# Kernel tuning notes

Measured on AMD Instinct MI355X. Metric: run time of the kernel, lower is better.

Reference implementation:

```python
import jax, jax.numpy as jnp
import numpy as np

PI = float(np.pi)
BN_EPS = 1e-3
LN_EPS = 1e-5


def ssslu(x, shape, bias):
    # x * (sin(softsign(x) * shape*pi/2) + (bias + 1))
    s = x / (1.0 + jnp.abs(x))
    return x * (jnp.sin(s * (shape * PI / 2.0)) + (bias + 1.0))


def bn(x, g, b, m, v):
    inv = (g / jnp.sqrt(v + BN_EPS))[None, :, None, None]
    return (x - m[None, :, None, None]) * inv + b[None, :, None, None]


def conv2d(x, w, bias=None, pad=0):
    y = jax.lax.conv_general_dilated(x, w, (1, 1), [(pad, pad), (pad, pad)],
                                     dimension_numbers=('NCHW', 'OIHW', 'NCHW'))
    if bias is not None:
        y = y + bias[None, :, None, None]
    return y


def ln_silu(v):
    # LayerNorm (unit weight, zero bias) over last axis, then SiLU
    mu = jnp.mean(v, axis=-1, keepdims=True)
    var = jnp.mean(jnp.square(v - mu), axis=-1, keepdims=True)
    h = (v - mu) / jnp.sqrt(var + LN_EPS)
    return h * jax.nn.sigmoid(h)


def _forward(x, w_qkv, g_qkv, b_qkv, m_qkv, v_qkv,
             w_co, g_co, b_co, m_co, v_co,
             w_b1, bias_b1, g_b1, b_b1, m_b1, v_b1,
             w_b2, bias_b2, g_b2, b_b2, m_b2, v_b2):
    B, C, H, W = x.shape
    Q = (w_qkv.shape[0] - C) // 2
    # qkv Conv block: conv1x1 -> SSSLU(-3, 0.3) -> BN
    t = bn(ssslu(conv2d(x, w_qkv, pad=0), -3.0, 0.3), g_qkv, b_qkv, m_qkv, v_qkv)
    xq, xk, xv = jnp.split(t, [Q, 2 * Q], axis=1)
    # max-pooled Q/K rows and columns -> [B*Q, W] / [B*Q, H]
    qw = jnp.max(xq, axis=2).reshape(B * Q, W)
    kw = jnp.max(xk, axis=2).reshape(B * Q, W)
    qh = jnp.max(xq, axis=3).reshape(B * Q, H)
    kh = jnp.max(xk, axis=3).reshape(B * Q, H)
    # xaw[i,b] = max_a qw[i,a]*kw[i,b]; xah[i,a] = max_b qh[i,a]*kh[i,b]
    xaw = jnp.max(qw[:, :, None] * kw[:, None, :], axis=1)  # [BQ, W]
    xah = jnp.max(qh[:, :, None] * kh[:, None, :], axis=2)  # [BQ, H]
    xaw = ln_silu(xaw)
    xah = ln_silu(xah)
    xa = (xah[:, :, None] * xaw[:, None, :]).reshape(B, Q, H, W)
    # co: SSSLUConv(Q+C -> Q): conv3x3 -> BN -> SSSLU(1.0, 0)
    xa = jnp.concatenate([xa, xv], axis=1)
    xa = ssslu(bn(conv2d(xa, w_co, pad=1), g_co, b_co, m_co, v_co), 1.0, 0.0)
    # back[0]: Conv(Q -> C, k3, bias): conv -> SSSLU(-3, 0.3) -> BN
    xa = bn(ssslu(conv2d(xa, w_b1, bias_b1, pad=1), -3.0, 0.3), g_b1, b_b1, m_b1, v_b1)
    # back[1]: SSSLUConv(C -> C, k1, bias): conv -> BN -> SSSLU(0.8, 0)
    xa = ssslu(bn(conv2d(xa, w_b2, bias_b2, pad=0), g_b2, b_b2, m_b2, v_b2), 0.8, 0.0)
    # back[2]: Sigmoid; source returns the gate itself
    return jax.nn.sigmoid(xa)


def setup_inputs() -> dict:
    B, C, Q, H, W = 16, 256, 256, 64, 64
    key = jax.random.key(0)
    ks = jax.random.split(key, 32)

    def w_init(k, o, i, kh, kw):
        return jax.random.normal(k, (o, i, kh, kw), jnp.float32) * (1.0 / np.sqrt(i * kh * kw))

    def bn_params(k, c):
        k1, k2, k3, k4 = jax.random.split(k, 4)
        g = jax.random.uniform(k1, (c,), jnp.float32, 0.5, 1.5)
        b = jax.random.normal(k2, (c,), jnp.float32) * 0.1
        m = jax.random.normal(k3, (c,), jnp.float32) * 0.1
        v = jax.random.uniform(k4, (c,), jnp.float32, 0.5, 1.5)
        return g, b, m, v

    x = jax.random.normal(ks[0], (B, C, H, W), jnp.float32)
    w_qkv = w_init(ks[1], 2 * Q + C, C, 1, 1)
    g_qkv, b_qkv, m_qkv, v_qkv = bn_params(ks[2], 2 * Q + C)
    w_co = w_init(ks[3], Q, Q + C, 3, 3)
    g_co, b_co, m_co, v_co = bn_params(ks[4], Q)
    w_b1 = w_init(ks[5], C, Q, 3, 3)
    bias_b1 = jax.random.normal(ks[6], (C,), jnp.float32) * 0.05
    g_b1, b_b1, m_b1, v_b1 = bn_params(ks[7], C)
    w_b2 = w_init(ks[8], C, C, 1, 1)
    bias_b2 = jax.random.normal(ks[9], (C,), jnp.float32) * 0.05
    g_b2, b_b2, m_b2, v_b2 = bn_params(ks[10], C)
    return dict(x=x, w_qkv=w_qkv, g_qkv=g_qkv, b_qkv=b_qkv, m_qkv=m_qkv, v_qkv=v_qkv,
                w_co=w_co, g_co=g_co, b_co=b_co, m_co=m_co, v_co=v_co,
                w_b1=w_b1, bias_b1=bias_b1, g_b1=g_b1, b_b1=b_b1, m_b1=m_b1, v_b1=v_b1,
                w_b2=w_b2, bias_b2=bias_b2, g_b2=g_b2, b_b2=b_b2, m_b2=m_b2, v_b2=v_b2)


def reference(x, w_qkv, g_qkv, b_qkv, m_qkv, v_qkv,
              w_co, g_co, b_co, m_co, v_co,
              w_b1, bias_b1, g_b1, b_b1, m_b1, v_b1,
              w_b2, bias_b2, g_b2, b_b2, m_b2, v_b2):
    return _forward(x, w_qkv, g_qkv, b_qkv, m_qkv, v_qkv,
                    w_co, g_co, b_co, m_co, v_co,
                    w_b1, bias_b1, g_b1, b_b1, m_b1, v_b1,
                    w_b2, bias_b2, g_b2, b_b2, m_b2, v_b2)
```

## Files before the change

kernel.cpp:

```cpp
#include <hip/hip_runtime.h>
#include <hip/hip_bf16.h>
#include <math.h>

#define PI_F 3.14159265358979323846f

typedef unsigned short u16;
typedef unsigned int   u32;
typedef float    f32x4 __attribute__((ext_vector_type(4)));
typedef _Float16 f16x8 __attribute__((ext_vector_type(8)));
typedef u16      u16x8 __attribute__((ext_vector_type(8)));
typedef u16      u16x4 __attribute__((ext_vector_type(4)));

__device__ __forceinline__ u16 f2h(float f){ union{ _Float16 h; u16 u; } c; c.h = (_Float16)f; return c.u; }
__device__ __forceinline__ float h2f(u16 u){ union{ u16 u; _Float16 h; } c; c.u = u; return (float)c.h; }

__device__ __forceinline__ void gl16(const void* g, void* l){
  __builtin_amdgcn_global_load_lds((const __attribute__((address_space(1))) u32*)g,
                                   (__attribute__((address_space(3))) u32*)l, 16, 0, 0);
}

__device__ __forceinline__ int SWZ(int r){ return (r>>1)&3; }

__device__ __forceinline__ float wred_max(float v){
#pragma unroll
  for (int m = 32; m; m >>= 1) v = fmaxf(v, __shfl_xor(v, m));
  return v;
}
__device__ __forceinline__ float wred_min(float v){
#pragma unroll
  for (int m = 32; m; m >>= 1) v = fminf(v, __shfl_xor(v, m));
  return v;
}
__device__ __forceinline__ float wred_sum(float v){
#pragma unroll
  for (int m = 32; m; m >>= 1) v += __shfl_xor(v, m);
  return v;
}

__device__ __forceinline__ float ssslu_f(float x, float shp, float bp1){
  float s = x / (1.0f + fabsf(x));
  return x * (__sinf(s * shp) + bp1);
}

__device__ __forceinline__ float epi_val(float v, float4 p, float shp, float bp1, int ORDER, bool SIG){
  v += p.w;
  if (ORDER == 0){ v = ssslu_f(v, shp, bp1); v = (v - p.z) * p.x + p.y; }
  else           { v = (v - p.z) * p.x + p.y; v = ssslu_f(v, shp, bp1); }
  if (SIG) v = 1.f / (1.f + __expf(-v));
  return v;
}

__device__ __forceinline__ f16x8 mul8h(u16x8 a, u16x8 b){
  union{ u16x8 u; f16x8 h; } A, B; A.u = a; B.u = b;
  return A.h * B.h;
}

__global__ __launch_bounds__(256)
void xpose_k(const float* __restrict__ X, u16* __restrict__ XH)
{
  __shared__ u16 L[16384];
  const int tid = threadIdx.x;
  const int b = blockIdx.x >> 6, h = blockIdx.x & 63;
  const float* xp = X + (size_t)b * 256 * 4096 + h * 64;
#pragma unroll
  for (int i = 0; i < 16; ++i){
    int ci = i * 16 + (tid >> 4);
    int w4 = (tid & 15) * 4;
    float4 v = *(const float4*)(xp + (size_t)ci * 4096 + w4);
    int sw = 4 * ((ci >> 3) & 15);
    u16x4 d;
    d[0] = f2h(v.x); d[1] = f2h(v.y); d[2] = f2h(v.z); d[3] = f2h(v.w);
    *(u16x4*)&L[ci * 64 + (w4 ^ sw)] = d;
  }
  __syncthreads();
  u16* out = XH + (((size_t)b * 4096 + (size_t)h * 64) << 8);
#pragma unroll
  for (int it = 0; it < 8; ++it){
    int w   = it * 8 + (tid >> 5);
    int m   = tid & 31;
    int ci0 = m * 8;
    int base = (w & ~3) ^ (4 * (m & 15));
    int wl   = w & 3;
    u16x8 o;
#pragma unroll
    for (int k = 0; k < 8; ++k)
      o[k] = L[(ci0 + k) * 64 + base + wl];
    *(u16x8*)&out[w * 256 + ci0] = o;
  }
}

template<int CI_T, bool CAT>
__global__ __launch_bounds__(256, 2)
void conv3_mfma(const u16* __restrict__ Apk, const u16* __restrict__ Bg,
                u16* __restrict__ DstH, const float4* __restrict__ pp,
                const u16* __restrict__ xahT_, const u16* __restrict__ xawT_,
                float shp, float bp1, int ORDER)
{
  constexpr int NCC = CI_T / 32;
  constexpr int NIT = NCC * 3;
  __shared__ __align__(16) u16 sAB[36864];

  const int tid  = threadIdx.x;
  const int lane = tid & 63;
  const int wv   = tid >> 6;
  const int wn   = wv;
  const int l15  = lane & 15, l4 = lane >> 4;

  const int bx  = blockIdx.x;
  const int bid = (bx & 7) * 32 + (bx >> 3);
  const int b   = bid >> 4;
  const int r0  = (bid & 15) * 4;
  const int m0  = blockIdx.y * 128;

  auto STAGE_A = [&](int it2){
    int d2 = it2 % 3, c2 = it2 / 3;
    int bufA = it2 & 1;
#pragma unroll
    for (int j2 = 0; j2 < 3; ++j2){
      int tap = d2 * 3 + j2;
      const u16* base = Apk + (size_t)tap * 256 * CI_T + (size_t)m0 * CI_T + c2 * 32;
#pragma unroll
      for (int i = 0; i < 2; ++i){
        int row = i * 64 + (tid >> 2);
        int s   = tid & 3;
        const u16* src = base + (size_t)row * CI_T + ((s ^ SWZ(row)) << 3);
        gl16(src, &sAB[bufA * 12288 + j2 * 4096 + (i * 64 + wv * 16) * 32]);
      }
    }
  };
  auto STAGE_B = [&](int c2){
#pragma unroll
    for (int j = 0; j < 6; ++j){
      int rr  = j;
      int hh  = r0 - 1 + rr; hh = min(63, max(0, hh));
      int w   = tid >> 2, s = tid & 3;
      int ci0 = c2 * 32 + ((s ^ SWZ(w + 1)) << 3);
      if (CAT && c2 < 8){
        u16x8 vh = *(const u16x8*)&xahT_[((b * 64 + hh) << 8) + ci0];
        u16x8 vw = *(const u16x8*)&xawT_[((b * 64 + w ) << 8) + ci0];
        *(f16x8*)&sAB[24576 + rr * 2048 + w * 32 + s * 8] = mul8h(vh, vw);
      } else {
        int ci = CAT ? (ci0 - 256) : ci0;
        const u16* src = Bg + (((size_t)b * 4096 + hh * 64 + w) << 8) + ci;
        gl16(src, &sAB[24576 + rr * 2048 + wv * 512]);
      }
    }
  };

  f32x4 acc[8][4];
#pragma unroll
  for (int i = 0; i < 8; ++i)
#pragma unroll
    for (int j = 0; j < 4; ++j){ acc[i][j][0]=0.f; acc[i][j][1]=0.f; acc[i][j][2]=0.f; acc[i][j][3]=0.f; }

  STAGE_A(0);

  for (int it = 0; it < NIT; ++it){
    const int d = it % 3, c = it / 3;
    const int bufA = it & 1;

    if (it + 1 < NIT) STAGE_A(it + 1);
    if (d == 0){
      STAGE_B(c);
      __syncthreads();
    }

    const int brow = wn + d;
    const bool rowok = ((unsigned)(r0 + wn + d - 1)) < 64u;

#pragma unroll
    for (int dw = 0; dw < 3; ++dw){
      f16x8 afr[8], bfr[4];
#pragma unroll
      for (int fm = 0; fm < 8; ++fm){
        int m  = fm * 16 + l15;
        int sl = l4 ^ SWZ(m);
        afr[fm] = *(const f16x8*)&sAB[bufA * 12288 + dw * 4096 + m * 32 + sl * 8];
      }
#pragma unroll
      for (int fn = 0; fn < 4; ++fn){
        int w_in = fn * 16 + l15 + dw - 1;
        int wc   = min(63, max(0, w_in));
        int sl2  = l4 ^ SWZ(wc + 1);
        f16x8 t  = *(const f16x8*)&sAB[24576 + brow * 2048 + wc * 32 + sl2 * 8];
        bool ok  = rowok && (((unsigned)w_in) < 64u);
        bfr[fn]  = ok ? t : (f16x8)(_Float16)0;
      }
      __builtin_amdgcn_s_setprio(1);
#pragma unroll
      for (int fm = 0; fm < 8; ++fm)
#pragma unroll
        for (int fn = 0; fn < 4; ++fn)
          acc[fm][fn] = __builtin_amdgcn_mfma_f32_16x16x32_f16(afr[fm], bfr[fn], acc[fm][fn], 0, 0, 0);
      __builtin_amdgcn_s_setprio(0);
    }
    __syncthreads();
  }

  const int h = r0 + wn;
#pragma unroll
  for (int fm = 0; fm < 8; ++fm){
    const int cobase = m0 + fm * 16 + 4 * l4;
    float4 P0 = pp[cobase], P1 = pp[cobase+1], P2 = pp[cobase+2], P3 = pp[cobase+3];
#pragma unroll
    for (int fn = 0; fn < 4; ++fn){
      int w = fn * 16 + l15;
      float v0 = epi_val(acc[fm][fn][0], P0, shp, bp1, ORDER, false);
      float v1 = epi_val(acc[fm][fn][1], P1, shp, bp1, ORDER, false);
      float v2 = epi_val(acc[fm][fn][2], P2, shp, bp1, ORDER, false);
      float v3 = epi_val(acc[fm][fn][3], P3, shp, bp1, ORDER, false);
      uint2 st;
      st.x = (u32)f2h(v0) | ((u32)f2h(v1) << 16);
      st.y = (u32)f2h(v2) | ((u32)f2h(v3) << 16);
      *(uint2*)&DstH[(((size_t)b * 4096 + (size_t)h * 64 + w) << 8) + cobase] = st;
    }
  }
}

template<int EPI>
__global__ __launch_bounds__(512, 2)
void conv1_big(const u16* __restrict__ Apk, const u16* __restrict__ Bg,
               u16* __restrict__ DstH, float* __restrict__ DstF,
               const float4* __restrict__ pp,
               float shp, float bp1, int ORDER)
{
  __shared__ __align__(16) u16 sA[2][8192];
  __shared__ __align__(16) u16 sB[2][8192];

  const int tid  = threadIdx.x;
  const int lane = tid & 63;
  const int wv   = tid >> 6;
  const int wm   = wv >> 2;
  const int wn   = wv & 3;
  const int l15  = lane & 15, l4 = lane >> 4;

  const int bx  = blockIdx.x;
  const int bid = (bx & 7) * 32 + (bx >> 3);
  const int b   = bid >> 4;
  const int h0  = (bid & 15) * 4;

  auto STAGE = [&](int c){
    int buf = c & 1;
#pragma unroll
    for (int j = 0; j < 2; ++j){
      int g = j * 512 + tid;
      int m = g >> 2, s = g & 3;
      const u16* srcA = Apk + (size_t)m * 256 + c * 32 + ((s ^ SWZ(m)) << 3);
      gl16(srcA, &sA[buf][(j * 512 + wv * 64) * 8]);
      int r = g >> 8, w = (g >> 2) & 63;
      const u16* srcB = Bg + (((size_t)b * 4096 + (h0 + r) * 64 + w) << 8) + c * 32 + ((s ^ SWZ(w)) << 3);
      gl16(srcB, &sB[buf][(j * 512 + wv * 64) * 8]);
    }
  };

  f32x4 acc[8][4];
#pragma unroll
  for (int i = 0; i < 8; ++i)
#pragma unroll
    for (int j = 0; j < 4; ++j){ acc[i][j][0]=0.f; acc[i][j][1]=0.f; acc[i][j][2]=0.f; acc[i][j][3]=0.f; }

  STAGE(0);
  __syncthreads();

  for (int c = 0; c < 8; ++c){
    if (c + 1 < 8) STAGE(c + 1);
    const int buf = c & 1;
    f16x8 afr[8], bfr[4];
#pragma unroll
    for (int fm = 0; fm < 8; ++fm){
      int m  = wm * 128 + fm * 16 + l15;
      int sl = l4 ^ SWZ(m);
      afr[fm] = *(const f16x8*)&sA[buf][m * 32 + sl * 8];
    }
#pragma unroll
    for (int fn = 0; fn < 4; ++fn){
      int w  = fn * 16 + l15;
      int sl = l4 ^ SWZ(w);
      bfr[fn] = *(const f16x8*)&sB[buf][(wn * 64 + w) * 32 + sl * 8];
    }
    __builtin_amdgcn_s_setprio(1);
#pragma unroll
    for (int fm = 0; fm < 8; ++fm)
#pragma unroll
      for (int fn = 0; fn < 4; ++fn)
        acc[fm][fn] = __builtin_amdgcn_mfma_f32_16x16x32_f16(afr[fm], bfr[fn], acc[fm][fn], 0, 0, 0);
    __builtin_amdgcn_s_setprio(0);
    __syncthreads();
  }

  const int h = h0 + wn;
#pragma unroll
  for (int fm = 0; fm < 8; ++fm){
    const int cobase = wm * 128 + fm * 16 + 4 * l4;
    float4 P0 = pp[cobase], P1 = pp[cobase+1], P2 = pp[cobase+2], P3 = pp[cobase+3];
#pragma unroll
    for (int fn = 0; fn < 4; ++fn){
      int w = fn * 16 + l15;
      if (EPI == 1){
        float v0 = epi_val(acc[fm][fn][0], P0, shp, bp1, ORDER, false);
        float v1 = epi_val(acc[fm][fn][1], P1, shp, bp1, ORDER, false);
        float v2 = epi_val(acc[fm][fn][2], P2, shp, bp1, ORDER, false);
        float v3 = epi_val(acc[fm][fn][3], P3, shp, bp1, ORDER, false);
        uint2 st;
        st.x = (u32)f2h(v0) | ((u32)f2h(v1) << 16);
        st.y = (u32)f2h(v2) | ((u32)f2h(v3) << 16);
        *(uint2*)&DstH[(((size_t)b * 4096 + (size_t)h * 64 + w) << 8) + cobase] = st;
      } else {
        float v0 = epi_val(acc[fm][fn][0], P0, shp, bp1, ORDER, true);
        float v1 = epi_val(acc[fm][fn][1], P1, shp, bp1, ORDER, true);
        float v2 = epi_val(acc[fm][fn][2], P2, shp, bp1, ORDER, true);
        float v3 = epi_val(acc[fm][fn][3], P3, shp, bp1, ORDER, true);
        size_t base = ((size_t)(b * 256 + cobase)) * 4096 + (size_t)h * 64 + w;
        DstF[base]          = v0;
        DstF[base + 4096]   = v1;
        DstF[base + 2*4096] = v2;
        DstF[base + 3*4096] = v3;
      }
    }
  }
}

__global__ __launch_bounds__(512, 2)
void conv1_pool(const u16* __restrict__ Apk0, const u16* __restrict__ Bg,
                const float4* __restrict__ pp0,
                float* __restrict__ qhp, float* __restrict__ khp,
                float* __restrict__ qwp, float* __restrict__ kwp,
                float shp, float bp1)
{
  __shared__ __align__(16) u16 S[32768];
  u16*   sA   = S;
  u16*   sB   = S + 16384;
  float* pool = (float*)S;

  const int tid  = threadIdx.x;
  const int lane = tid & 63;
  const int wv   = tid >> 6;
  const int wm   = wv >> 2;
  const int wn   = wv & 3;
  const int l15  = lane & 15, l4 = lane >> 4;

  const int bx   = blockIdx.x;
  const int bid  = (bx & 7) * 32 + (bx >> 3);
  const int b    = bid >> 4;
  const int hblk = bid & 15;
  const int h0   = hblk * 4;
  const int m0   = blockIdx.y * 256;

  const u16*    Apk = Apk0 + (size_t)m0 * 256;
  const float4* pp  = pp0 + m0;
  float* rowp = (blockIdx.y == 0) ? qhp : khp;
  float* colp = (blockIdx.y == 0) ? qwp : kwp;

  auto STAGE = [&](int c){
    int buf = c & 1;
#pragma unroll
    for (int j = 0; j < 2; ++j){
      int g = j * 512 + tid;
      int m = g >> 2, s = g & 3;
      const u16* srcA = Apk + (size_t)m * 256 + c * 32 + ((s ^ SWZ(m)) << 3);
      gl16(srcA, &sA[buf * 8192 + (j * 512 + wv * 64) * 8]);
      int r = g >> 8, w = (g >> 2) & 63;
      const u16* srcB = Bg + (((size_t)b * 4096 + (h0 + r) * 64 + w) << 8) + c * 32 + ((s ^ SWZ(w)) << 3);
      gl16(srcB, &sB[buf * 8192 + (j * 512 + wv * 64) * 8]);
    }
  };

  f32x4 acc[8][4];
#pragma unroll
  for (int i = 0; i < 8; ++i)
#pragma unroll
    for (int j = 0; j < 4; ++j){ acc[i][j][0]=0.f; acc[i][j][1]=0.f; acc[i][j][2]=0.f; acc[i][j][3]=0.f; }

  STAGE(0);
  __syncthreads();

  for (int c = 0; c < 8; ++c){
    if (c + 1 < 8) STAGE(c + 1);
    const int buf = c & 1;
    f16x8 afr[8], bfr[4];
#pragma unroll
    for (int fm = 0; fm < 8; ++fm){
      int m  = wm * 128 + fm * 16 + l15;
      int sl = l4 ^ SWZ(m);
      afr[fm] = *(const f16x8*)&sA[buf * 8192 + m * 32 + sl * 8];
    }
#pragma unroll
    for (int fn = 0; fn < 4; ++fn){
      int w  = fn * 16 + l15;
      int sl = l4 ^ SWZ(w);
      bfr[fn] = *(const f16x8*)&sB[buf * 8192 + (wn * 64 + w) * 32 + sl * 8];
    }
    __builtin_amdgcn_s_setprio(1);
#pragma unroll
    for (int fm = 0; fm < 8; ++fm)
#pragma unroll
      for (int fn = 0; fn < 4; ++fn)
        acc[fm][fn] = __builtin_amdgcn_mfma_f32_16x16x32_f16(afr[fm], bfr[fn], acc[fm][fn], 0, 0, 0);
    __builtin_amdgcn_s_setprio(0);
    __syncthreads();
  }

  const int h = h0 + wn;
#pragma unroll
  for (int k = 0; k < 4; ++k){
    if (wn == k){
#pragma unroll
      for (int fm = 0; fm < 8; ++fm){
        const int cl = wm * 128 + fm * 16 + 4 * l4;
        float4 P0 = pp[cl], P1 = pp[cl+1], P2 = pp[cl+2], P3 = pp[cl+3];
        float ev[4][4];
#pragma unroll
        for (int fn = 0; fn < 4; ++fn){
          ev[fn][0] = epi_val(acc[fm][fn][0], P0, shp, bp1, 0, false);
          ev[fn][1] = epi_val(acc[fm][fn][1], P1, shp, bp1, 0, false);
          ev[fn][2] = epi_val(acc[fm][fn][2], P2, shp, bp1, 0, false);
          ev[fn][3] = epi_val(acc[fm][fn][3], P3, shp, bp1, 0, false);
        }
#pragma unroll
        for (int r = 0; r < 4; ++r){
          float mv = fmaxf(fmaxf(ev[0][r], ev[1][r]), fmaxf(ev[2][r], ev[3][r]));
          mv = fmaxf(mv, __shfl_xor(mv, 1));
          mv = fmaxf(mv, __shfl_xor(mv, 2));
          mv = fmaxf(mv, __shfl_xor(mv, 4));
          mv = fmaxf(mv, __shfl_xor(mv, 8));
          if (l15 == 0)
            rowp[(((b << 8) | (cl + r)) << 6) + h] = mv;
        }
#pragma unroll
        for (int fn = 0; fn < 4; ++fn)
#pragma unroll
          for (int r = 0; r < 4; ++r){
            int idx = ((cl + r) << 6) + fn * 16 + l15;
            pool[idx] = (k == 0) ? ev[fn][r] : fmaxf(pool[idx], ev[fn][r]);
          }
      }
    }
    __syncthreads();
  }
  float* cbase = colp + (((size_t)(b * 16 + hblk)) << 14);
#pragma unroll
  for (int j = 0; j < 8; ++j){
    int fi = j * 512 + tid;
    *(float4*)&cbase[fi * 4] = *(const float4*)&pool[fi * 4];
  }
}

__device__ __forceinline__ float ln_silu_wave(float v){
  float mu = wred_sum(v) * (1.f / 64.f);
  float d = v - mu;
  float var = wred_sum(d * d) * (1.f / 64.f);
  float hn = d * rsqrtf(var + 1e-5f);
  return hn / (1.f + __expf(-hn));
}

__global__ void attn_k(const float* __restrict__ qwp, const float* __restrict__ kwp,
                       const float* __restrict__ qh, const float* __restrict__ kh,
                       u16* __restrict__ xahT, u16* __restrict__ xawT)
{
  int row  = blockIdx.x * 4 + (threadIdx.x >> 6);
  int lane = threadIdx.x & 63;
  int idx  = (row << 6) + lane;
  int b = row >> 8, q = row & 255;
  size_t pb = ((size_t)b << 18) + (q << 6) + lane;
  float qwv = -3.0e38f, kwv = -3.0e38f;
#pragma unroll
  for (int hb = 0; hb < 16; ++hb){
    qwv = fmaxf(qwv, qwp[pb + ((size_t)hb << 14)]);
    kwv = fmaxf(kwv, kwp[pb + ((size_t)hb << 14)]);
  }
  float qhv = qh[idx], khv = kh[idx];
  float Pq = wred_max(qwv), mq = wred_min(qwv);
  float Pk = wred_max(khv), mk = wred_min(khv);
  float aw = fmaxf(kwv * Pq, kwv * mq);
  float ah = fmaxf(qhv * Pk, qhv * mk);
  aw = ln_silu_wave(aw);
  ah = ln_silu_wave(ah);
  xawT[((b * 64 + lane) << 8) + q] = f2h(aw);
  xahT[((b * 64 + lane) << 8) + q] = f2h(ah);
}

__global__ void pack_k(const float* __restrict__ wqkv, const float* __restrict__ wco,
                       const float* __restrict__ wb1, const float* __restrict__ wb2,
                       const float* gq, const float* bq, const float* mq, const float* vq,
                       const float* gc, const float* bc, const float* mc, const float* vc,
                       const float* g1, const float* b1, const float* m1, const float* v1, const float* bias1,
                       const float* g2, const float* b2, const float* m2, const float* v2, const float* bias2,
                       u16* __restrict__ WQ, u16* __restrict__ WCO, u16* __restrict__ WB1, u16* __restrict__ WB2,
                       float4* __restrict__ PP)
{
  const int E0 = 196608, E1 = 196608 + 1179648, E2 = 196608 + 1179648 + 589824, E3 = 2031616;
  int i = blockIdx.x * 256 + threadIdx.x;
  if (i >= E3 + 1536) return;
  if (i < E0){ WQ[i] = f2h(wqkv[i]); }
  else if (i < E1){
    int d = i - E0; int tap = d / 131072; int rm = d % 131072; int m = rm >> 9; int ci = rm & 511;
    WCO[d] = f2h(wco[(size_t)((m << 9) | ci) * 9 + tap]);
  } else if (i < E2){
    int d = i - E1; int tap = d / 65536; int rm = d & 65535; int m = rm >> 8; int ci = rm & 255;
    WB1[d] = f2h(wb1[(size_t)((m << 8) | ci) * 9 + tap]);
  } else if (i < E3){
    int d = i - E2; WB2[d] = f2h(wb2[d]);
  } else {
    int c = i - E3;
    float g, be, mm, vv, bi;
    if (c < 768){ g = gq[c]; be = bq[c]; mm = mq[c]; vv = vq[c]; bi = 0.f; }
    else if (c < 1024){ int j = c - 768;  g = gc[j]; be = bc[j]; mm = mc[j]; vv = vc[j]; bi = 0.f; }
    else if (c < 1280){ int j = c - 1024; g = g1[j]; be = b1[j]; mm = m1[j]; vv = v1[j]; bi = bias1[j]; }
    else              { int j = c - 1280; g = g2[j]; be = b2[j]; mm = m2[j]; vv = v2[j]; bi = bias2[j]; }
    PP[c] = make_float4(g / sqrtf(vv + 1e-3f), be, mm, bi);
  }
}

extern "C" void kernel_launch(void* const* d_in, const int* in_sizes, int n_in,
                              void* d_out, int out_size, void* d_ws, size_t ws_size,
                              hipStream_t stream)
{
  const float* x       = (const float*)d_in[0];
  const float* w_qkv   = (const float*)d_in[1];
  const float* g_qkv   = (const float*)d_in[2];
  const float* b_qkv   = (const float*)d_in[3];
  const float* m_qkv   = (const float*)d_in[4];
  const float* v_qkv   = (const float*)d_in[5];
  const float* w_co    = (const float*)d_in[6];
  const float* g_co    = (const float*)d_in[7];
  const float* b_co    = (const float*)d_in[8];
  const float* m_co    = (const float*)d_in[9];
  const float* v_co    = (const float*)d_in[10];
  const float* w_b1    = (const float*)d_in[11];
  const float* bias_b1 = (const float*)d_in[12];
  const float* g_b1    = (const float*)d_in[13];
  const float* b_b1    = (const float*)d_in[14];
  const float* m_b1    = (const float*)d_in[15];
  const float* v_b1    = (const float*)d_in[16];
  const float* w_b2    = (const float*)d_in[17];
  const float* bias_b2 = (const float*)d_in[18];
  const float* g_b2    = (const float*)d_in[19];
  const float* b_b2    = (const float*)d_in[20];
  const float* m_b2    = (const float*)d_in[21];
  const float* v_b2    = (const float*)d_in[22];
  float* out = (float*)d_out;

  char* W = (char*)d_ws;
  u16*    WQ   = (u16*)(W + 0);
  u16*    WCO  = (u16*)(W + 393216);
  u16*    WB1  = (u16*)(W + 2752512);
  u16*    WB2  = (u16*)(W + 3932160);
  float4* PP   = (float4*)(W + 4063232);
  float*  qwp_ = (float*)(W + 4087808);
  float*  kwp_ = (float*)(W + 20865024);
  u16*    TV   = (u16*)(W + 4087808);
  u16*    XAHT = (u16*)(W + 37642240);
  u16*    XAWT = (u16*)(W + 38166528);
  u16*    XH   = (u16*)(W + 38690816);
  u16*    Y1   = (u16*)(W + 38690816);
  u16*    Y2   = TV;
  float*  qh_  = (float*)(W + 72245248);
  float*  kh_  = (float*)(W + 73293824);

  const size_t NEED = 74342400;
  if (ws_size < NEED) return;

  const float SHP_N3 = -3.0f * PI_F * 0.5f;
  const float SHP_1  =  1.0f * PI_F * 0.5f;
  const float SHP_08 =  0.8f * PI_F * 0.5f;

  dim3 blk(256);

  pack_k<<<7942, blk, 0, stream>>>(w_qkv, w_co, w_b1, w_b2,
      g_qkv, b_qkv, m_qkv, v_qkv,
      g_co,  b_co,  m_co,  v_co,
      g_b1,  b_b1,  m_b1,  v_b1,  bias_b1,
      g_b2,  b_b2,  m_b2,  v_b2,  bias_b2,
      WQ, WCO, WB1, WB2, PP);

  xpose_k<<<1024, blk, 0, stream>>>(x, XH);

  conv1_pool<<<dim3(256, 2), 512, 0, stream>>>(
      WQ, XH, PP, qh_, kh_, qwp_, kwp_, SHP_N3, 1.3f);

  attn_k<<<1024, blk, 0, stream>>>(qwp_, kwp_, qh_, kh_, XAHT, XAWT);

  conv1_big<1><<<256, 512, 0, stream>>>(
      WQ + (size_t)512 * 256, XH, TV, nullptr, PP + 512, SHP_N3, 1.3f, 0);

  conv3_mfma<512, true><<<dim3(256, 2), blk, 0, stream>>>(
      WCO, TV, Y1, PP + 768, XAHT, XAWT, SHP_1, 1.0f, 1);

  conv3_mfma<256, false><<<dim3(256, 2), blk, 0, stream>>>(
      WB1, Y1, Y2, PP + 1024, nullptr, nullptr, SHP_N3, 1.3f, 0);

  conv1_big<2><<<256, 512, 0, stream>>>(
      WB2, Y2, nullptr, out, PP + 1280, SHP_08, 1.0f, 1);
}
```

Before: 450.0 us.

## Pad conv3x3 LDS B tile with zero halo and precompute fragment addresses

```diff
diff --git a/kernel.cpp b/kernel.cpp
--- a/kernel.cpp
+++ b/kernel.cpp
@@ -98,7 +98,7 @@
 {
   constexpr int NCC = CI_T / 32;
   constexpr int NIT = NCC * 3;
-  __shared__ __align__(16) u16 sAB[36864];
+  __shared__ __align__(16) u16 sAB[37248];
 
   const int tid  = threadIdx.x;
   const int lane = tid & 63;
@@ -112,37 +112,47 @@
   const int r0  = (bid & 15) * 4;
   const int m0  = blockIdx.y * 128;
 
+  if (tid < 192){
+    int rr = tid >> 5, rem = tid & 31;
+    int wp = (rem & 16) ? 65 : 0;
+    *(u32*)&sAB[24576 + rr * 2112 + wp * 32 + (rem & 15) * 2] = 0;
+  }
+  if (r0 == 0)
+    for (int i = tid; i < 1056; i += 256) *(u32*)&sAB[24576 + i * 2] = 0;
+  if (r0 == 60)
+    for (int i = tid; i < 1056; i += 256) *(u32*)&sAB[24576 + 5 * 2112 + i * 2] = 0;
+
+  const int rA = tid >> 2, s4 = tid & 3;
+  const u32 offA0 = ((u32)rA * CI_T + ((s4 ^ SWZ(rA)) << 3)) * 2;
+  const u32 offA1 = ((u32)(rA + 64) * CI_T + ((s4 ^ SWZ(rA + 64)) << 3)) * 2;
+  const u32 offB  = (((u32)rA << 8) + ((s4 ^ SWZ(rA + 1)) << 3)) * 2;
+
   auto STAGE_A = [&](int it2){
     int d2 = it2 % 3, c2 = it2 / 3;
-    int bufA = it2 & 1;
+    u16* dst = &sAB[(it2 & 1) * 12288 + wv * 512];
+    const char* pa = (const char*)(Apk + ((size_t)(d2 * 3 * 256) + m0) * CI_T + c2 * 32);
 #pragma unroll
     for (int j2 = 0; j2 < 3; ++j2){
-      int tap = d2 * 3 + j2;
-      const u16* base = Apk + (size_t)tap * 256 * CI_T + (size_t)m0 * CI_T + c2 * 32;
-#pragma unroll
-      for (int i = 0; i < 2; ++i){
-        int row = i * 64 + (tid >> 2);
-        int s   = tid & 3;
-        const u16* src = base + (size_t)row * CI_T + ((s ^ SWZ(row)) << 3);
-        gl16(src, &sAB[bufA * 12288 + j2 * 4096 + (i * 64 + wv * 16) * 32]);
-      }
+      gl16(pa + offA0, dst + j2 * 4096);
+      gl16(pa + offA1, dst + j2 * 4096 + 2048);
+      pa += (size_t)256 * CI_T * 2;
     }
   };
   auto STAGE_B = [&](int c2){
 #pragma unroll
     for (int j = 0; j < 6; ++j){
-      int rr  = j;
-      int hh  = r0 - 1 + rr; hh = min(63, max(0, hh));
-      int w   = tid >> 2, s = tid & 3;
-      int ci0 = c2 * 32 + ((s ^ SWZ(w + 1)) << 3);
+      int hh = r0 - 1 + j;
+      if ((unsigned)hh >= 64u) continue;
       if (CAT && c2 < 8){
+        int w = rA, s = s4;
+        int ci0 = c2 * 32 + ((s ^ SWZ(w + 1)) << 3);
         u16x8 vh = *(const u16x8*)&xahT_[((b * 64 + hh) << 8) + ci0];
         u16x8 vw = *(const u16x8*)&xawT_[((b * 64 + w ) << 8) + ci0];
-        *(f16x8*)&sAB[24576 + rr * 2048 + w * 32 + s * 8] = mul8h(vh, vw);
+        *(f16x8*)&sAB[24576 + j * 2112 + (w + 1) * 32 + s * 8] = mul8h(vh, vw);
       } else {
-        int ci = CAT ? (ci0 - 256) : ci0;
-        const u16* src = Bg + (((size_t)b * 4096 + hh * 64 + w) << 8) + ci;
-        gl16(src, &sAB[24576 + rr * 2048 + wv * 512]);
+        int cio = CAT ? (c2 * 32 - 256) : (c2 * 32);
+        const char* pb = (const char*)(Bg + (((size_t)b * 4096 + (size_t)hh * 64) << 8) + cio);
+        gl16(pb + offB, &sAB[24576 + j * 2112 + 32 + wv * 512]);
       }
     }
   };
@@ -153,48 +163,45 @@
 #pragma unroll
     for (int j = 0; j < 4; ++j){ acc[i][j][0]=0.f; acc[i][j][1]=0.f; acc[i][j][2]=0.f; acc[i][j][3]=0.f; }
 
+  const char* lds = (const char*)sAB;
+  const u32 aoff = (u32)l15 * 64 + (u32)((l4 ^ ((l15 >> 1) & 3)) << 4);
+  const char* ab0 = lds + aoff;
+  const char* ab1 = lds + aoff + 24576;
+  const u32 bcom = 49152u + (u32)wn * 4224;
+  const char* bb0 = lds + bcom + (u32)(l15 + 0) * 64 + (u32)((l4 ^ (((l15 + 0) >> 1) & 3)) << 4);
+  const char* bb1 = lds + bcom + (u32)(l15 + 1) * 64 + (u32)((l4 ^ (((l15 + 1) >> 1) & 3)) << 4);
+  const char* bb2 = lds + bcom + (u32)(l15 + 2) * 64 + (u32)((l4 ^ (((l15 + 2) >> 1) & 3)) << 4);
+
   STAGE_A(0);
 
-  for (int it = 0; it < NIT; ++it){
-    const int d = it % 3, c = it / 3;
-    const int bufA = it & 1;
-
-    if (it + 1 < NIT) STAGE_A(it + 1);
-    if (d == 0){
-      STAGE_B(c);
+  for (int c = 0; c < NCC; ++c){
+#pragma unroll
+    for (int d = 0; d < 3; ++d){
+      const int it = 3 * c + d;
+      if (it + 1 < NIT) STAGE_A(it + 1);
+      if (d == 0){ STAGE_B(c); __syncthreads(); }
+
+      const char* ab = ((c + d) & 1) ? ab1 : ab0;
+#pragma unroll
+      for (int dw = 0; dw < 3; ++dw){
+        const char* bp = (dw == 0) ? bb0 : (dw == 1) ? bb1 : bb2;
+        f16x8 afr[8], bfr[4];
+#pragma unroll
+        for (int fm = 0; fm < 8; ++fm)
+          afr[fm] = *(const f16x8*)(ab + dw * 8192 + fm * 1024);
+#pragma unroll
+        for (int fn = 0; fn < 4; ++fn)
+          bfr[fn] = *(const f16x8*)(bp + d * 4224 + fn * 1024);
+        __builtin_amdgcn_s_setprio(1);
+#pragma unroll
+        for (int fm = 0; fm < 8; ++fm)
+#pragma unroll
+          for (int fn = 0; fn < 4; ++fn)
+            acc[fm][fn] = __builtin_amdgcn_mfma_f32_16x16x32_f16(afr[fm], bfr[fn], acc[fm][fn], 0, 0, 0);
+        __builtin_amdgcn_s_setprio(0);
+      }
       __syncthreads();
     }
-
-    const int brow = wn + d;
-    const bool rowok = ((unsigned)(r0 + wn + d - 1)) < 64u;
-
-#pragma unroll
-    for (int dw = 0; dw < 3; ++dw){
-      f16x8 afr[8], bfr[4];
-#pragma unroll
-      for (int fm = 0; fm < 8; ++fm){
-        int m  = fm * 16 + l15;
-        int sl = l4 ^ SWZ(m);
-        afr[fm] = *(const f16x8*)&sAB[bufA * 12288 + dw * 4096 + m * 32 + sl * 8];
-      }
-#pragma unroll
-      for (int fn = 0; fn < 4; ++fn){
-        int w_in = fn * 16 + l15 + dw - 1;
-        int wc   = min(63, max(0, w_in));
-        int sl2  = l4 ^ SWZ(wc + 1);
-        f16x8 t  = *(const f16x8*)&sAB[24576 + brow * 2048 + wc * 32 + sl2 * 8];
-        bool ok  = rowok && (((unsigned)w_in) < 64u);
-        bfr[fn]  = ok ? t : (f16x8)(_Float16)0;
-      }
-      __builtin_amdgcn_s_setprio(1);
-#pragma unroll
-      for (int fm = 0; fm < 8; ++fm)
-#pragma unroll
-        for (int fn = 0; fn < 4; ++fn)
-          acc[fm][fn] = __builtin_amdgcn_mfma_f32_16x16x32_f16(afr[fm], bfr[fn], acc[fm][fn], 0, 0, 0);
-      __builtin_amdgcn_s_setprio(0);
-    }
-    __syncthreads();
   }
 
   const int h = r0 + wn;
```

Result: faster. 433.8 us (-3.6%).
